# Performance work log

Measured on AMD Instinct MI355X. Metric: run time of the kernel, lower is better.

## Reference

```python
import jax, jax.numpy as jnp
import numpy as np

CUTOFF = 32.0  # matches init_kwargs cutoff


def _reduce_single(elem, cutoff):
    """elem: [T, D]. Returns (means_padded [T, D], n_segs scalar int32).

    Faithful to the torch loop: representative = elem[0]; walk frames; when
    ||rep - frame|| > cutoff, close the segment [rep_id:f_ind] (mean over it)
    and restart at `frame`. Final open segment is also emitted. Because the
    number of segments is data-dependent, we return a fixed-shape [T, D]
    buffer whose first n_segs rows are the stacked segment means (rest zeros).
    """
    T, D = elem.shape

    def step(rep, frame):
        d = jnp.linalg.norm(rep - frame)  # torch.norm default = Frobenius/L2
        new_seg = d > cutoff
        rep = jnp.where(new_seg, frame, rep)
        return rep, new_seg

    # flags[i] == True means frame i+1 starts a new segment
    _, flags = jax.lax.scan(step, elem[0], elem[1:])
    flags = jnp.concatenate([jnp.zeros((1,), dtype=bool), flags])  # frame 0 never starts anew
    seg_id = jnp.cumsum(flags.astype(jnp.int32))  # [T], ordered segment ids
    n_segs = seg_id[-1] + 1

    sums = jax.ops.segment_sum(elem, seg_id, num_segments=T)  # [T, D]
    counts = jax.ops.segment_sum(jnp.ones((T,), elem.dtype), seg_id, num_segments=T)  # [T]
    means = sums / jnp.maximum(counts, 1.0)[:, None]  # padded rows stay 0
    return means, n_segs


def setup_inputs() -> dict:
    key = jax.random.key(0)
    batch = jax.random.normal(key, (16, 4096, 512), dtype=jnp.float32)
    return {"batch": batch}


def reference(batch):
    # vmap over the list-of-sequences batch dim (all sequences same length T)
    means, n_segs = jax.vmap(lambda e: _reduce_single(e, CUTOFF))(batch)
    return means, n_segs
```

## Files before the change

kernel.cpp:

```cpp
#include <hip/hip_runtime.h>

#define NB 16
#define NT 4096
#define ND 512
#define NLEV 12

typedef float f4v __attribute__((ext_vector_type(4)));

__device__ __forceinline__ bool decide_exact(const float* __restrict__ base, int row,
                                             int lane, float4 r0, float4 r1) {
    const float4* fp = (const float4*)(base + (size_t)row * ND);
    float4 y0 = fp[lane];
    float4 y1 = fp[lane + 64];
    float d;
    double sd;
    d = r0.x - y0.x; sd  = (double)d * d;
    d = r0.y - y0.y; sd += (double)d * d;
    d = r0.z - y0.z; sd += (double)d * d;
    d = r0.w - y0.w; sd += (double)d * d;
    d = r1.x - y1.x; sd += (double)d * d;
    d = r1.y - y1.y; sd += (double)d * d;
    d = r1.z - y1.z; sd += (double)d * d;
    d = r1.w - y1.w; sd += (double)d * d;
    #pragma unroll
    for (int off = 32; off >= 1; off >>= 1) sd += __shfl_xor(sd, off, 64);
    return ((float)sd > 1024.0f);
}

__global__ __launch_bounds__(256) void kA_next(const float* __restrict__ in,
                                               int* __restrict__ nxt) {
    int L = (blockIdx.x & 7) * 2048 + (blockIdx.x >> 3);
    int wave = L * 4 + (threadIdx.x >> 6);
    int lane = threadIdx.x & 63;
    int b = wave >> 12;
    int j = wave & (NT - 1);
    int g = lane >> 4;
    int q = lane & 15;

    const float* base = in + (size_t)b * NT * ND;
    const float4* jrow = (const float4*)(base + (size_t)j * ND);
    float4 rep[8];
    #pragma unroll
    for (int k = 0; k < 8; ++k) rep[k] = jrow[q + 16 * k];

    int result = NT;
    int i = j + 1;
    while (i < NT) {
        int row = i + g;
        bool valid = row < NT;
        int rc = valid ? row : NT - 1;
        const float4* pr = (const float4*)(base + (size_t)rc * ND);
        float s = 0.f;
        #pragma unroll
        for (int k = 0; k < 8; ++k) {
            float4 x = pr[q + 16 * k];
            float d;
            d = rep[k].x - x.x; s = fmaf(d, d, s);
            d = rep[k].y - x.y; s = fmaf(d, d, s);
            d = rep[k].z - x.z; s = fmaf(d, d, s);
            d = rep[k].w - x.w; s = fmaf(d, d, s);
        }
        s += __shfl_xor(s, 1, 64);
        s += __shfl_xor(s, 2, 64);
        s += __shfl_xor(s, 4, 64);
        s += __shfl_xor(s, 8, 64);

        unsigned long long ym = __ballot(q == 0 && valid && s > 1024.25f);
        unsigned long long am = __ballot(q == 0 && valid && s > 1023.75f && s <= 1024.25f);
        unsigned vy = (unsigned)((ym & 1ull) | ((ym >> 15) & 2ull) |
                                 ((ym >> 30) & 4ull) | ((ym >> 45) & 8ull));
        unsigned va = (unsigned)((am & 1ull) | ((am >> 15) & 2ull) |
                                 ((am >> 30) & 4ull) | ((am >> 45) & 8ull));
        int found = -1;
        for (;;) {
            int gy = vy ? (__ffs(vy) - 1) : 4;
            int ga = va ? (__ffs(va) - 1) : 4;
            if (ga < gy) {
                float4 r0 = jrow[lane];
                float4 r1 = jrow[lane + 64];
                if (decide_exact(base, i + ga, lane, r0, r1)) { found = i + ga; break; }
                va &= va - 1;
            } else {
                if (gy < 4) found = i + gy;
                break;
            }
        }
        if (found >= 0) { result = found; break; }
        i += 4;
    }
    if (lane == 0) nxt[b * NT + j] = result;
}

__global__ __launch_bounds__(1024) void kChain(const int* __restrict__ nxt,
                                               int* __restrict__ start,
                                               int* __restrict__ nseg,
                                               float* __restrict__ out_tail) {
    __shared__ unsigned short h[NT + 1];
    __shared__ unsigned short h2[NT + 1];
    __shared__ unsigned reach[NT / 32];
    __shared__ unsigned pref[NT / 32];
    int b = blockIdx.x;
    int t = threadIdx.x;
    for (int j = t; j <= NT; j += 1024)
        h[j] = (j < NT) ? (unsigned short)nxt[b * NT + j] : (unsigned short)NT;
    for (int w = t; w < NT / 32; w += 1024) reach[w] = 0;
    __syncthreads();
    if (t == 0) reach[0] = 1u;
    __syncthreads();
    for (int k = 0; k < NLEV; ++k) {
        #pragma unroll
        for (int j = t; j < NT; j += 1024) {
            if (reach[j >> 5] & (1u << (j & 31))) {
                int d = h[j];
                if (d < NT) atomicOr(&reach[d >> 5], 1u << (d & 31));
            }
        }
        __syncthreads();
        for (int j = t; j <= NT; j += 1024) h2[j] = h[h[j]];
        __syncthreads();
        for (int j = t; j <= NT; j += 1024) h[j] = h2[j];
        __syncthreads();
    }
    if (t < NT / 32) pref[t] = __popc(reach[t]);
    __syncthreads();
    for (int off = 1; off < NT / 32; off <<= 1) {
        unsigned v = 0;
        if (t < NT / 32 && t >= off) v = pref[t - off];
        __syncthreads();
        if (t < NT / 32) pref[t] += v;
        __syncthreads();
    }
    int n = pref[NT / 32 - 1];
    for (int j = t; j < NT; j += 1024) {
        unsigned w = reach[j >> 5];
        if (w & (1u << (j & 31))) {
            int r = (int)(pref[j >> 5] - __popc(w) + __popc(w & ((1u << (j & 31)) - 1)));
            start[b * NT + r] = j;
        }
    }
    if (t == 0) { nseg[b] = n; out_tail[b] = (float)n; }
}

__global__ __launch_bounds__(256) void kD_means(const float* __restrict__ in,
                                                const int* __restrict__ nxt,
                                                const int* __restrict__ start,
                                                const int* __restrict__ nseg,
                                                float* __restrict__ out) {
    int wave = blockIdx.x * 4 + (threadIdx.x >> 6);
    int lane = threadIdx.x & 63;
    int b = wave >> 12;
    int r = wave & (NT - 1);
    float4 acc0 = make_float4(0.f, 0.f, 0.f, 0.f);
    float4 acc1 = make_float4(0.f, 0.f, 0.f, 0.f);
    int n = nseg[b];
    if (r < n) {
        int s = start[b * NT + r];
        int e = nxt[b * NT + s];
        const float4* base = (const float4*)(in + (size_t)(b * NT + s) * ND);
        int cnt = e - s;
        int f = 0;
        for (; f + 2 <= cnt; f += 2) {
            float4 v0 = base[(size_t)f * (ND / 4) + lane];
            float4 v1 = base[(size_t)f * (ND / 4) + lane + 64];
            float4 w0 = base[(size_t)(f + 1) * (ND / 4) + lane];
            float4 w1 = base[(size_t)(f + 1) * (ND / 4) + lane + 64];
            acc0.x += v0.x + w0.x; acc0.y += v0.y + w0.y;
            acc0.z += v0.z + w0.z; acc0.w += v0.w + w0.w;
            acc1.x += v1.x + w1.x; acc1.y += v1.y + w1.y;
            acc1.z += v1.z + w1.z; acc1.w += v1.w + w1.w;
        }
        if (f < cnt) {
            float4 v0 = base[(size_t)f * (ND / 4) + lane];
            float4 v1 = base[(size_t)f * (ND / 4) + lane + 64];
            acc0.x += v0.x; acc0.y += v0.y; acc0.z += v0.z; acc0.w += v0.w;
            acc1.x += v1.x; acc1.y += v1.y; acc1.z += v1.z; acc1.w += v1.w;
        }
        float c = (float)cnt;
        acc0.x /= c; acc0.y /= c; acc0.z /= c; acc0.w /= c;
        acc1.x /= c; acc1.y /= c; acc1.z /= c; acc1.w /= c;
    }
    f4v* orow = (f4v*)(out + (size_t)(b * NT + r) * ND);
    f4v o0 = {acc0.x, acc0.y, acc0.z, acc0.w};
    f4v o1 = {acc1.x, acc1.y, acc1.z, acc1.w};
    __builtin_nontemporal_store(o0, &orow[lane]);
    __builtin_nontemporal_store(o1, &orow[lane + 64]);
}

extern "C" void kernel_launch(void* const* d_in, const int* in_sizes, int n_in,
                              void* d_out, int out_size, void* d_ws, size_t ws_size,
                              hipStream_t stream) {
    const float* in = (const float*)d_in[0];
    float* out = (float*)d_out;
    char* ws = (char*)d_ws;

    int* nxt   = (int*)(ws + 0);
    int* start = (int*)(ws + 262144);
    int* nseg  = (int*)(ws + 524288);

    kA_next <<<16384, 256,  0, stream>>>(in, nxt);
    kChain  <<<NB,    1024, 0, stream>>>(nxt, start, nseg,
                                         out + (size_t)NB * NT * ND);
    kD_means<<<16384, 256,  0, stream>>>(in, nxt, start, nseg, out);
}
```

Baseline: 304.1 us.

## Tile next-break search in LDS: 32 reps per block share a 40-row window

The next-segment-break kernel now assigns 32 consecutive start rows to each block. It stages a 40-row window of input into shared memory, and each wave scans its reps against the shared window before falling back to global loads past the window. This is meant to cut redundant global/L2 traffic, since neighbouring reps re-read the same nearby rows. The cost is 80 KB of LDS per block, which limits occupancy, plus a serial loop of 8 reps per wave.

Result: slower. 337.5 us (+11.0%).

```diff
diff --git a/kernel.cpp b/kernel.cpp
--- a/kernel.cpp
+++ b/kernel.cpp
@@ -4,6 +4,8 @@
 #define NT 4096
 #define ND 512
 #define NLEV 12
+#define TILE 32
+#define WROWS 40
 
 typedef float f4v __attribute__((ext_vector_type(4)));
 
@@ -29,66 +31,134 @@
 
 __global__ __launch_bounds__(256) void kA_next(const float* __restrict__ in,
                                                int* __restrict__ nxt) {
-    int L = (blockIdx.x & 7) * 2048 + (blockIdx.x >> 3);
-    int wave = L * 4 + (threadIdx.x >> 6);
-    int lane = threadIdx.x & 63;
-    int b = wave >> 12;
-    int j = wave & (NT - 1);
-    int g = lane >> 4;
-    int q = lane & 15;
+    __shared__ float lds[WROWS * ND];
+    int tid  = threadIdx.x;
+    int j0g  = blockIdx.x * TILE;
+    int b    = j0g >> 12;
+    int j0   = j0g & (NT - 1);
+    int win  = min(WROWS, NT - j0);
 
     const float* base = in + (size_t)b * NT * ND;
-    const float4* jrow = (const float4*)(base + (size_t)j * ND);
-    float4 rep[8];
-    #pragma unroll
-    for (int k = 0; k < 8; ++k) rep[k] = jrow[q + 16 * k];
-
-    int result = NT;
-    int i = j + 1;
-    while (i < NT) {
-        int row = i + g;
-        bool valid = row < NT;
-        int rc = valid ? row : NT - 1;
-        const float4* pr = (const float4*)(base + (size_t)rc * ND);
-        float s = 0.f;
+
+    {
+        const float4* g4 = (const float4*)(base + (size_t)j0 * ND);
+        float4* l4w = (float4*)lds;
+        int elems4 = win * (ND / 4);
+        for (int idx = tid; idx < elems4; idx += 256) l4w[idx] = g4[idx];
+    }
+    __syncthreads();
+
+    int w    = tid >> 6;
+    int lane = tid & 63;
+    int g    = lane >> 4;
+    int q    = lane & 15;
+    const float4* l4 = (const float4*)lds;
+
+    for (int t = 0; t < 8; ++t) {
+        int jj = w + 4 * t;
+        int jl = j0 + jj;
+        const float4* jrowg = (const float4*)(base + (size_t)jl * ND);
+
+        float4 rep[8];
         #pragma unroll
-        for (int k = 0; k < 8; ++k) {
-            float4 x = pr[q + 16 * k];
-            float d;
-            d = rep[k].x - x.x; s = fmaf(d, d, s);
-            d = rep[k].y - x.y; s = fmaf(d, d, s);
-            d = rep[k].z - x.z; s = fmaf(d, d, s);
-            d = rep[k].w - x.w; s = fmaf(d, d, s);
-        }
-        s += __shfl_xor(s, 1, 64);
-        s += __shfl_xor(s, 2, 64);
-        s += __shfl_xor(s, 4, 64);
-        s += __shfl_xor(s, 8, 64);
-
-        unsigned long long ym = __ballot(q == 0 && valid && s > 1024.25f);
-        unsigned long long am = __ballot(q == 0 && valid && s > 1023.75f && s <= 1024.25f);
-        unsigned vy = (unsigned)((ym & 1ull) | ((ym >> 15) & 2ull) |
-                                 ((ym >> 30) & 4ull) | ((ym >> 45) & 8ull));
-        unsigned va = (unsigned)((am & 1ull) | ((am >> 15) & 2ull) |
-                                 ((am >> 30) & 4ull) | ((am >> 45) & 8ull));
+        for (int k = 0; k < 8; ++k) rep[k] = l4[jj * (ND / 4) + q + 16 * k];
+
         int found = -1;
-        for (;;) {
-            int gy = vy ? (__ffs(vy) - 1) : 4;
-            int ga = va ? (__ffs(va) - 1) : 4;
-            if (ga < gy) {
-                float4 r0 = jrow[lane];
-                float4 r1 = jrow[lane + 64];
-                if (decide_exact(base, i + ga, lane, r0, r1)) { found = i + ga; break; }
-                va &= va - 1;
-            } else {
-                if (gy < 4) found = i + gy;
-                break;
-            }
-        }
-        if (found >= 0) { result = found; break; }
-        i += 4;
-    }
-    if (lane == 0) nxt[b * NT + j] = result;
+        for (int br = jj + 1; br < win && found < 0; br += 4) {
+            int rr = br + g;
+            bool valid = rr < win;
+            int rc = valid ? rr : win - 1;
+            float s = 0.f;
+            #pragma unroll
+            for (int k = 0; k < 8; ++k) {
+                float4 x = l4[rc * (ND / 4) + q + 16 * k];
+                float d;
+                d = rep[k].x - x.x; s = fmaf(d, d, s);
+                d = rep[k].y - x.y; s = fmaf(d, d, s);
+                d = rep[k].z - x.z; s = fmaf(d, d, s);
+                d = rep[k].w - x.w; s = fmaf(d, d, s);
+            }
+            s += __shfl_xor(s, 1, 64);
+            s += __shfl_xor(s, 2, 64);
+            s += __shfl_xor(s, 4, 64);
+            s += __shfl_xor(s, 8, 64);
+
+            unsigned long long ym = __ballot(q == 0 && valid && s > 1024.25f);
+            unsigned long long am = __ballot(q == 0 && valid && s > 1023.75f && s <= 1024.25f);
+            unsigned vy = (unsigned)((ym & 1ull) | ((ym >> 15) & 2ull) |
+                                     ((ym >> 30) & 4ull) | ((ym >> 45) & 8ull));
+            unsigned va = (unsigned)((am & 1ull) | ((am >> 15) & 2ull) |
+                                     ((am >> 30) & 4ull) | ((am >> 45) & 8ull));
+            for (;;) {
+                int gy = vy ? (__ffs(vy) - 1) : 4;
+                int ga = va ? (__ffs(va) - 1) : 4;
+                if (ga < gy) {
+                    float4 r0 = jrowg[lane];
+                    float4 r1 = jrowg[lane + 64];
+                    if (decide_exact(base, j0 + br + ga, lane, r0, r1)) {
+                        found = j0 + br + ga; break;
+                    }
+                    va &= va - 1;
+                } else {
+                    if (gy < 4) found = j0 + br + gy;
+                    break;
+                }
+            }
+        }
+
+        int result;
+        if (found >= 0) {
+            result = found;
+        } else if (j0 + win >= NT) {
+            result = NT;
+        } else {
+            result = NT;
+            int i = j0 + win;
+            while (i < NT) {
+                int row = i + g;
+                bool valid = row < NT;
+                int rc = valid ? row : NT - 1;
+                const float4* pr = (const float4*)(base + (size_t)rc * ND);
+                float s = 0.f;
+                #pragma unroll
+                for (int k = 0; k < 8; ++k) {
+                    float4 x = pr[q + 16 * k];
+                    float d;
+                    d = rep[k].x - x.x; s = fmaf(d, d, s);
+                    d = rep[k].y - x.y; s = fmaf(d, d, s);
+                    d = rep[k].z - x.z; s = fmaf(d, d, s);
+                    d = rep[k].w - x.w; s = fmaf(d, d, s);
+                }
+                s += __shfl_xor(s, 1, 64);
+                s += __shfl_xor(s, 2, 64);
+                s += __shfl_xor(s, 4, 64);
+                s += __shfl_xor(s, 8, 64);
+                unsigned long long ym = __ballot(q == 0 && valid && s > 1024.25f);
+                unsigned long long am = __ballot(q == 0 && valid && s > 1023.75f && s <= 1024.25f);
+                unsigned vy = (unsigned)((ym & 1ull) | ((ym >> 15) & 2ull) |
+                                         ((ym >> 30) & 4ull) | ((ym >> 45) & 8ull));
+                unsigned va = (unsigned)((am & 1ull) | ((am >> 15) & 2ull) |
+                                         ((am >> 30) & 4ull) | ((am >> 45) & 8ull));
+                int f2 = -1;
+                for (;;) {
+                    int gy = vy ? (__ffs(vy) - 1) : 4;
+                    int ga = va ? (__ffs(va) - 1) : 4;
+                    if (ga < gy) {
+                        float4 r0 = jrowg[lane];
+                        float4 r1 = jrowg[lane + 64];
+                        if (decide_exact(base, i + ga, lane, r0, r1)) { f2 = i + ga; break; }
+                        va &= va - 1;
+                    } else {
+                        if (gy < 4) f2 = i + gy;
+                        break;
+                    }
+                }
+                if (f2 >= 0) { result = f2; break; }
+                i += 4;
+            }
+        }
+        if (lane == 0) nxt[b * NT + jl] = result;
+    }
 }
 
 __global__ __launch_bounds__(1024) void kChain(const int* __restrict__ nxt,
@@ -197,8 +267,8 @@
     int* start = (int*)(ws + 262144);
     int* nseg  = (int*)(ws + 524288);
 
-    kA_next <<<16384, 256,  0, stream>>>(in, nxt);
-    kChain  <<<NB,    1024, 0, stream>>>(nxt, start, nseg,
-                                         out + (size_t)NB * NT * ND);
-    kD_means<<<16384, 256,  0, stream>>>(in, nxt, start, nseg, out);
-}
+    kA_next <<<NB * NT / TILE, 256,  0, stream>>>(in, nxt);
+    kChain  <<<NB,             1024, 0, stream>>>(nxt, start, nseg,
+                                                  out + (size_t)NB * NT * ND);
+    kD_means<<<16384,          256,  0, stream>>>(in, nxt, start, nseg, out);
+}
```
